# Kernel tuning notes

Measured on AMD Instinct MI355X. Metric: run time of the kernel, lower is better.

The kernel has to match this reference:

```python
import jax, jax.numpy as jnp
from jax import lax
import numpy as np

TAPS = 4          # db2 filter length
LEVEL = 4
CH = 32
SLOPE = 10.0      # sigmoid sharpness of learned hard-threshold activation

# db2 decomposition low-pass coefficients (pywt convention)
_DB2 = np.array([-0.12940952255126037, 0.2241438680420134,
                 0.8365163037378079, 0.48296291314453416], dtype=np.float32)

def setup_inputs() -> dict:
    key = jax.random.key(0)
    k1, k2, k3 = jax.random.split(key, 3)
    x = jax.random.normal(k1, (128, CH, 4096), dtype=jnp.float32)
    # learned per-channel, per-level low-pass kernels: db2 init + small perturbation
    h_lo = jnp.asarray(_DB2)[None, None, :] + 0.02 * jax.random.normal(
        k2, (CH, LEVEL, TAPS), dtype=jnp.float32)
    # learned symmetric thresholds (Act_Init=0 -> small positive values)
    bias = 0.1 * jax.random.uniform(k3, (CH, LEVEL), dtype=jnp.float32)
    return {"x": x, "h_lo": h_lo, "bias": bias}

def _grouped_dwt_step(a, k_lo, k_hi):
    # a: [B,C,T]; kernels: [C,1,taps]; circular boundary, stride-2 downsample
    B, C, T = a.shape
    a_pad = jnp.concatenate([a, a[..., : TAPS - 1]], axis=-1)  # circular pad
    dn = ('NCH', 'OIH', 'NCH')
    lo = lax.conv_general_dilated(a_pad, k_lo, (2,), 'VALID',
                                  dimension_numbers=dn, feature_group_count=C)
    hi = lax.conv_general_dilated(a_pad, k_hi, (2,), 'VALID',
                                  dimension_numbers=dn, feature_group_count=C)
    return lo, hi  # each [B,C,T//2]

def reference(x, h_lo, bias):
    """Batched learned wavelet decomposition (all channels at once via grouped conv).
    Returns coefficients packed along last dim: [yl, d_L, ..., d_1] -> [B,C,T].
    """
    B, C, T = x.shape
    sign = ((-1.0) ** jnp.arange(TAPS)).astype(x.dtype)  # QMF sign flip
    a = x
    details = []
    for l in range(LEVEL):
        k_lo = h_lo[:, l, :][:, None, :]                       # [C,1,taps]
        k_hi = (sign * h_lo[:, l, ::-1])[:, None, :]           # high-pass via QMF
        a, hi = _grouped_dwt_step(a, k_lo, k_hi)
        b = bias[None, :, l, None]                             # [1,C,1]
        # symmetric sigmoid (soft hard-threshold) activation on detail coeffs
        d = hi * (jax.nn.sigmoid(SLOPE * (hi - b)) + jax.nn.sigmoid(-SLOPE * (hi + b)))
        details.append(d)
    # pack: approximation (coarsest) first, then details coarsest->finest
    return jnp.concatenate([a] + details[::-1], axis=-1)
```

## Files before the change

kernel.cpp:

```cpp
#include <hip/hip_runtime.h>
#include <math.h>

#define TLEN 4096
#define LEVELS 4
#define CHANS 32
#define SLOPE 10.0f

__device__ __forceinline__ float clamp30(float v) {
    return __builtin_amdgcn_fmed3f(v, -30.f, 30.f);
}

__device__ __forceinline__ float sgate(float hi, float b) {
    const float ea = __expf(clamp30(-SLOPE * (hi - b)));
    const float eb = __expf(clamp30( SLOPE * (hi + b)));
    return hi * (2.f + ea + eb) * __builtin_amdgcn_rcpf((1.f + ea) * (1.f + eb));
}

__global__ __launch_bounds__(256) void lwpt_kernel(
    const float* __restrict__ x, const float* __restrict__ h_lo,
    const float* __restrict__ bias, float* __restrict__ out)
{
    const int bc  = blockIdx.x;
    const int c   = bc & (CHANS - 1);
    const int tid = threadIdx.x;

    const float* xrow = x   + (size_t)bc * TLEN;
    float*       orow = out + (size_t)bc * TLEN;

    const float4 k0v = ((const float4*)h_lo)[c * LEVELS + 0];
    const float4 k1v = ((const float4*)h_lo)[c * LEVELS + 1];
    const float4 k2v = ((const float4*)h_lo)[c * LEVELS + 2];
    const float4 k3v = ((const float4*)h_lo)[c * LEVELS + 3];
    const float b0 = bias[c * LEVELS + 0];
    const float b1 = bias[c * LEVELS + 1];
    const float b2 = bias[c * LEVELS + 2];
    const float b3 = bias[c * LEVELS + 3];

    float in[46];
    const int base = 16 * tid;
    #pragma unroll
    for (int k = 0; k < 4; ++k) {
        const float4 v = *(const float4*)(xrow + base + 4 * k);
        in[4*k+0] = v.x; in[4*k+1] = v.y; in[4*k+2] = v.z; in[4*k+3] = v.w;
    }
    #pragma unroll
    for (int k = 0; k < 7; ++k) {
        const float4 v = *(const float4*)(xrow + ((base + 16 + 4 * k) & (TLEN - 1)));
        in[16+4*k+0] = v.x; in[16+4*k+1] = v.y; in[16+4*k+2] = v.z; in[16+4*k+3] = v.w;
    }
    {
        const float2 e = *(const float2*)(xrow + ((base + 44) & (TLEN - 1)));
        in[44] = e.x; in[45] = e.y;
    }

    float lo1[22];
    #pragma unroll
    for (int j = 0; j < 22; ++j)
        lo1[j] = in[2*j]*k0v.x + in[2*j+1]*k0v.y + in[2*j+2]*k0v.z + in[2*j+3]*k0v.w;
    {
        float dd[8];
        #pragma unroll
        for (int j = 0; j < 8; ++j) {
            const float hi = in[2*j]*k0v.w - in[2*j+1]*k0v.z + in[2*j+2]*k0v.y - in[2*j+3]*k0v.x;
            dd[j] = sgate(hi, b0);
        }
        float4* o4 = (float4*)(orow + 2048);
        o4[2*tid]   = make_float4(dd[0], dd[1], dd[2], dd[3]);
        o4[2*tid+1] = make_float4(dd[4], dd[5], dd[6], dd[7]);
    }

    float lo2[10];
    #pragma unroll
    for (int j = 0; j < 10; ++j)
        lo2[j] = lo1[2*j]*k1v.x + lo1[2*j+1]*k1v.y + lo1[2*j+2]*k1v.z + lo1[2*j+3]*k1v.w;
    {
        float dd[4];
        #pragma unroll
        for (int j = 0; j < 4; ++j) {
            const float hi = lo1[2*j]*k1v.w - lo1[2*j+1]*k1v.z + lo1[2*j+2]*k1v.y - lo1[2*j+3]*k1v.x;
            dd[j] = sgate(hi, b1);
        }
        ((float4*)(orow + 1024))[tid] = make_float4(dd[0], dd[1], dd[2], dd[3]);
    }

    float lo3[4];
    #pragma unroll
    for (int j = 0; j < 4; ++j)
        lo3[j] = lo2[2*j]*k2v.x + lo2[2*j+1]*k2v.y + lo2[2*j+2]*k2v.z + lo2[2*j+3]*k2v.w;
    {
        float dd[2];
        #pragma unroll
        for (int j = 0; j < 2; ++j) {
            const float hi = lo2[2*j]*k2v.w - lo2[2*j+1]*k2v.z + lo2[2*j+2]*k2v.y - lo2[2*j+3]*k2v.x;
            dd[j] = sgate(hi, b2);
        }
        ((float2*)(orow + 512))[tid] = make_float2(dd[0], dd[1]);
    }

    {
        const float lo = lo3[0]*k3v.x + lo3[1]*k3v.y + lo3[2]*k3v.z + lo3[3]*k3v.w;
        const float hi = lo3[0]*k3v.w - lo3[1]*k3v.z + lo3[2]*k3v.y - lo3[3]*k3v.x;
        orow[tid]       = lo;
        orow[256 + tid] = sgate(hi, b3);
    }
}

extern "C" void kernel_launch(void* const* d_in, const int* in_sizes, int n_in,
                              void* d_out, int out_size, void* d_ws, size_t ws_size,
                              hipStream_t stream) {
    const float* x    = (const float*)d_in[0];
    const float* h_lo = (const float*)d_in[1];
    const float* bias = (const float*)d_in[2];
    float* out = (float*)d_out;

    dim3 grid(128 * CHANS);
    dim3 block(256);
    lwpt_kernel<<<grid, block, 0, stream>>>(x, h_lo, bias, out);
}
```

Before: 29.14 us.

## Exchange level-2 approximations through shared memory to cut redundant halo recompute

Each thread previously loaded a 46-sample window and recomputed overlapping level-1 and level-2 lows for its neighbours. Now each thread loads only 22 samples, computes its own level-2 lows, writes them to shared memory, and after a block barrier reads neighbour values to finish levels 3 and 4. This cuts global halo loads, redundant FMAs and register pressure, at the cost of one __syncthreads and some LDS traffic.

```diff
diff --git a/kernel.cpp b/kernel.cpp
--- a/kernel.cpp
+++ b/kernel.cpp
@@ -20,6 +20,8 @@
     const float* __restrict__ x, const float* __restrict__ h_lo,
     const float* __restrict__ bias, float* __restrict__ out)
 {
+    __shared__ float bufB[1024];
+
     const int bc  = blockIdx.x;
     const int c   = bc & (CHANS - 1);
     const int tid = threadIdx.x;
@@ -36,27 +38,25 @@
     const float b2 = bias[c * LEVELS + 2];
     const float b3 = bias[c * LEVELS + 3];
 
-    float in[46];
+    float in[22];
     const int base = 16 * tid;
     #pragma unroll
     for (int k = 0; k < 4; ++k) {
         const float4 v = *(const float4*)(xrow + base + 4 * k);
         in[4*k+0] = v.x; in[4*k+1] = v.y; in[4*k+2] = v.z; in[4*k+3] = v.w;
     }
-    #pragma unroll
-    for (int k = 0; k < 7; ++k) {
-        const float4 v = *(const float4*)(xrow + ((base + 16 + 4 * k) & (TLEN - 1)));
-        in[16+4*k+0] = v.x; in[16+4*k+1] = v.y; in[16+4*k+2] = v.z; in[16+4*k+3] = v.w;
-    }
     {
-        const float2 e = *(const float2*)(xrow + ((base + 44) & (TLEN - 1)));
-        in[44] = e.x; in[45] = e.y;
+        const float4 v = *(const float4*)(xrow + ((base + 16) & (TLEN - 1)));
+        in[16] = v.x; in[17] = v.y; in[18] = v.z; in[19] = v.w;
+        const float2 e = *(const float2*)(xrow + ((base + 20) & (TLEN - 1)));
+        in[20] = e.x; in[21] = e.y;
     }
 
-    float lo1[22];
+    float lo1[10];
     #pragma unroll
-    for (int j = 0; j < 22; ++j)
+    for (int j = 0; j < 10; ++j)
         lo1[j] = in[2*j]*k0v.x + in[2*j+1]*k0v.y + in[2*j+2]*k0v.z + in[2*j+3]*k0v.w;
+
     {
         float dd[8];
         #pragma unroll
@@ -69,35 +69,44 @@
         o4[2*tid+1] = make_float4(dd[4], dd[5], dd[6], dd[7]);
     }
 
-    float lo2[10];
-    #pragma unroll
-    for (int j = 0; j < 10; ++j)
-        lo2[j] = lo1[2*j]*k1v.x + lo1[2*j+1]*k1v.y + lo1[2*j+2]*k1v.z + lo1[2*j+3]*k1v.w;
     {
-        float dd[4];
+        float lo[4], dd[4];
         #pragma unroll
         for (int j = 0; j < 4; ++j) {
-            const float hi = lo1[2*j]*k1v.w - lo1[2*j+1]*k1v.z + lo1[2*j+2]*k1v.y - lo1[2*j+3]*k1v.x;
+            const float a0 = lo1[2*j], a1 = lo1[2*j+1], a2 = lo1[2*j+2], a3 = lo1[2*j+3];
+            lo[j] = a0*k1v.x + a1*k1v.y + a2*k1v.z + a3*k1v.w;
+            const float hi = a0*k1v.w - a1*k1v.z + a2*k1v.y - a3*k1v.x;
             dd[j] = sgate(hi, b1);
         }
+        ((float4*)bufB)[tid] = make_float4(lo[0], lo[1], lo[2], lo[3]);
         ((float4*)(orow + 1024))[tid] = make_float4(dd[0], dd[1], dd[2], dd[3]);
     }
-
-    float lo3[4];
-    #pragma unroll
-    for (int j = 0; j < 4; ++j)
-        lo3[j] = lo2[2*j]*k2v.x + lo2[2*j+1]*k2v.y + lo2[2*j+2]*k2v.z + lo2[2*j+3]*k2v.w;
-    {
-        float dd[2];
-        #pragma unroll
-        for (int j = 0; j < 2; ++j) {
-            const float hi = lo2[2*j]*k2v.w - lo2[2*j+1]*k2v.z + lo2[2*j+2]*k2v.y - lo2[2*j+3]*k2v.x;
-            dd[j] = sgate(hi, b2);
-        }
-        ((float2*)(orow + 512))[tid] = make_float2(dd[0], dd[1]);
-    }
+    __syncthreads();
 
     {
+        float t10[10];
+        const float4 v0 = ((const float4*)bufB)[tid];
+        const float4 v1 = *(const float4*)(bufB + ((4 * tid + 4) & 1023));
+        const float2 e  = *(const float2*)(bufB + ((4 * tid + 8) & 1023));
+        t10[0] = v0.x; t10[1] = v0.y; t10[2] = v0.z; t10[3] = v0.w;
+        t10[4] = v1.x; t10[5] = v1.y; t10[6] = v1.z; t10[7] = v1.w;
+        t10[8] = e.x;  t10[9] = e.y;
+
+        float lo3[4];
+        #pragma unroll
+        for (int j = 0; j < 4; ++j)
+            lo3[j] = t10[2*j]*k2v.x + t10[2*j+1]*k2v.y + t10[2*j+2]*k2v.z + t10[2*j+3]*k2v.w;
+
+        {
+            float dd[2];
+            #pragma unroll
+            for (int j = 0; j < 2; ++j) {
+                const float hi = t10[2*j]*k2v.w - t10[2*j+1]*k2v.z + t10[2*j+2]*k2v.y - t10[2*j+3]*k2v.x;
+                dd[j] = sgate(hi, b2);
+            }
+            ((float2*)(orow + 512))[tid] = make_float2(dd[0], dd[1]);
+        }
+
         const float lo = lo3[0]*k3v.x + lo3[1]*k3v.y + lo3[2]*k3v.z + lo3[3]*k3v.w;
         const float hi = lo3[0]*k3v.w - lo3[1]*k3v.z + lo3[2]*k3v.y - lo3[3]*k3v.x;
         orow[tid]       = lo;
```

New measurement: 28.60 us. No clear change (-1.8%).
